# Performance work log

Measured on AMD Instinct MI355X. Metric: run time of the kernel, lower is better.

The kernel has to match this reference:

```python
import jax, jax.numpy as jnp
import numpy as np

B, N, D = 2, 2048, 128
DEPTH, RECURRENCE = 3, 3
EDGE_P = 0.03  # Bernoulli edge density -> avg degree ~61


def _p(key, shape, fan_in):
    return jax.random.normal(key, shape, dtype=jnp.float32) / np.float32(np.sqrt(fan_in))


def setup_inputs() -> dict:
    key = jax.random.key(0)
    ks = jax.random.split(key, 6)
    node = jax.random.normal(ks[0], (B, N, 1), dtype=jnp.float32)
    A = (jax.random.uniform(ks[1], (B, N, N)) < EDGE_P).astype(jnp.float32)
    edge = jax.random.uniform(ks[2], (B, N, N), dtype=jnp.float32) + 0.1  # strictly positive edge weights
    inp = {"node": node, "edge": edge, "A": A}
    # (fan_in, heads) per attention layer; last layer hardcodes heads=2, concat=False
    specs = [(1, 1), (D, 1), (D, 2)]
    for l, (fin, H) in enumerate(specs):
        kk = jax.random.split(ks[3 + l], 5)
        inp[f"Wq{l}"] = _p(kk[0], (fin, H, D), fin)
        inp[f"Wk{l}"] = _p(kk[1], (fin, H, D), fin)
        inp[f"Wv{l}"] = _p(kk[2], (fin, H, D), fin)
        inp[f"We{l}"] = _p(kk[3], (H, D), 1)  # lin_edge: edge_dim=1 -> H*D, stored as (H, D)
        inp[f"Ws{l}"] = _p(kk[4], (fin, H * D if l < DEPTH - 1 else D), fin)  # root/skip lin
    return inp


def _layer_norm(x, eps=1e-5):
    mu = x.mean(-1, keepdims=True)
    var = ((x - mu) ** 2).mean(-1, keepdims=True)
    return (x - mu) / jnp.sqrt(var + eps)


def _tconv(x, e_t, mask, Wq, Wk, Wv, We, Ws, concat):
    # PyG TransformerConv (bias removed, root_weight=True):
    #   alpha_ij = softmax_j( q_i . (k_j + W_e e_ij) / sqrt(d) ) over in-neighbors j of i
    #   out_i = sum_j alpha_ij (v_j + W_e e_ij)  (+ W_skip x_i)
    # e_ij is a scalar so W_e e_ij = e_ij * We, a rank-1 term we never materialize per-edge.
    # x: (b,n,fin); e_t[b,dst,src]; We: (H,d)
    H, d = We.shape
    q = jnp.einsum('bnf,fhd->bnhd', x, Wq)
    k = jnp.einsum('bnf,fhd->bnhd', x, Wk)
    v = jnp.einsum('bnf,fhd->bnhd', x, Wv)
    scores = jnp.einsum('bihd,bjhd->bhij', q, k)  # i=dst, j=src
    qe = jnp.einsum('bihd,hd->bhi', q, We)
    scores = (scores + qe[..., None] * e_t[:, None]) / np.float32(np.sqrt(d))
    scores = jnp.where(mask[:, None], scores, jnp.finfo(scores.dtype).min)
    alpha = jax.nn.softmax(scores, axis=-1)
    alpha = jnp.where(mask[:, None], alpha, 0.0)  # isolated dst nodes aggregate to zero
    out = jnp.einsum('bhij,bjhd->bihd', alpha, v)
    ew = jnp.einsum('bhij,bij->bhi', alpha, e_t)  # sum_j alpha * e_ij
    out = out + ew.transpose(0, 2, 1)[..., None] * We
    out = out.reshape(x.shape[0], x.shape[1], H * d) if concat else out.mean(axis=2)
    return out + x @ Ws


def reference(node, edge, A, Wq0, Wk0, Wv0, We0, Ws0, Wq1, Wk1, Wv1, We1, Ws1, Wq2, Wk2, Wv2, We2, Ws2):
    e = edge * A
    e_t = jnp.swapaxes(e, 1, 2)  # e_t[b, dst, src]  (edge_index: row=src, col=dst)
    mask = e_t != 0  # dense_to_sparse keeps nonzero entries
    layers = [
        (Wq0, Wk0, Wv0, We0, Ws0, True),
        (Wq1, Wk1, Wv1, We1, Ws1, True),
        (Wq2, Wk2, Wv2, We2, Ws2, False),
    ]
    emb = node
    for r in range(RECURRENCE):
        for l in range(DEPTH):
            if r != 0 and l == 0:
                continue
            Wq, Wk, Wv, We, Ws, concat = layers[l]
            emb = _tconv(emb, e_t, mask, Wq, Wk, Wv, We, Ws, concat)
            if l != DEPTH - 1:
                emb = jax.nn.relu(_layer_norm(emb))
    return emb  # (b, n, out_dim[-1])
```

## Files before the change

### kernel.cpp

```cpp
#include <hip/hip_runtime.h>
#include <hip/hip_bf16.h>

#define BB 2
#define NN 2048
#define DD 128
#define BN (BB*NN)
#define CAP 128
#define TD 16
#define QSTR 256
#define SSTR 128
#define INV_SQRT_D 0.08838834764831845f

typedef __attribute__((ext_vector_type(8))) short short8;
typedef __attribute__((ext_vector_type(4))) float f32x4;

__device__ inline float b2f(unsigned short u) {
    union { unsigned int i; float f; } c; c.i = (unsigned int)u << 16; return c.f;
}
__device__ inline float b2f_hi(unsigned int raw) {
    union { unsigned int i; float f; } c; c.i = raw & 0xffff0000u; return c.f;
}
__device__ inline float b2f_lo(unsigned int raw) {
    union { unsigned int i; float f; } c; c.i = raw << 16; return c.f;
}

__global__ __launch_bounds__(256) void prep(
    const float* __restrict__ A, const float* __restrict__ edge,
    const float* __restrict__ node,
    const float* __restrict__ Wq0, const float* __restrict__ Wk0,
    const float* __restrict__ Wv0, const float* __restrict__ Ws0,
    const float* __restrict__ Wq1, const float* __restrict__ Wk1,
    const float* __restrict__ Wv1, const float* __restrict__ Ws1,
    const float* __restrict__ Wq2, const float* __restrict__ Wk2,
    const float* __restrict__ Wv2, const float* __restrict__ Ws2,
    __hip_bfloat16* __restrict__ Wt1, __hip_bfloat16* __restrict__ Wt2,
    float* __restrict__ q, __hip_bfloat16* __restrict__ kA,
    __hip_bfloat16* __restrict__ vA, float* __restrict__ s,
    int* __restrict__ deg, unsigned short* __restrict__ cols,
    float* __restrict__ evals)
{
    __shared__ int   cnt[TD];
    __shared__ int   csh[TD][CAP];
    __shared__ float esh[TD][CAP];
    __shared__ float xnode[16];

    int bid = blockIdx.x;
    int tid = threadIdx.x;

    if (bid < 256) {
        int b    = bid >> 7;
        int dst0 = (bid & 127) * TD;

        if (tid < TD) cnt[tid] = 0;
        __syncthreads();

        int srcOff = tid >> 2;
        int dOff   = (tid & 3) * 4;
        const size_t base = (size_t)b * NN * NN + dst0 + dOff;

#pragma unroll 2
        for (int s0 = 0; s0 < NN; s0 += 64) {
            int src = s0 + srcOff;
            float4 a4 = *(const float4*)&A[base + (size_t)src * NN];
            float4 e4 = *(const float4*)&edge[base + (size_t)src * NN];
            int gsrc = b * NN + src;
            float av[4] = {a4.x, a4.y, a4.z, a4.w};
            float ev[4] = {e4.x, e4.y, e4.z, e4.w};
#pragma unroll
            for (int u = 0; u < 4; u++) {
                if (av[u] != 0.f) {
                    int d = dOff + u;
                    int slot = atomicAdd(&cnt[d], 1);
                    if (slot < CAP) { csh[d][slot] = gsrc; esh[d][slot] = ev[u] * av[u]; }
                }
            }
        }
        __syncthreads();

        if (tid < TD) deg[b * NN + dst0 + tid] = min(cnt[tid], CAP);
        for (int idx = tid; idx < TD * CAP; idx += 256) {
            int d = idx / CAP, i = idx % CAP;
            if (i < min(cnt[d], CAP)) {
                size_t row = (size_t)(b * NN + dst0 + d);
                cols [row * CAP + i] = (unsigned short)csh[d][i];
                evals[row * CAP + i] = esh[d][i];
            }
        }
    } else if (bid < 256 + 1408) {
        int c = bid - 256;
        if (tid < DD) {
            const float *Wq, *Wk, *Wv, *Ws; __hip_bfloat16* Wt; int n, HD;
            if (c < 512) { Wq = Wq1; Wk = Wk1; Wv = Wv1; Ws = Ws1; Wt = Wt1; n = c;       HD = DD;     }
            else         { Wq = Wq2; Wk = Wk2; Wv = Wv2; Ws = Ws2; Wt = Wt2; n = c - 512; HD = 2 * DD; }
            const float* src; int ld; int col;
            if      (n < HD)     { src = Wq; col = n;          ld = HD; }
            else if (n < 2*HD)   { src = Wk; col = n - HD;     ld = HD; }
            else if (n < 3*HD)   { src = Wv; col = n - 2*HD;   ld = HD; }
            else                 { src = Ws; col = n - 3*HD;   ld = DD; }
            Wt[(size_t)n * DD + tid] = __float2bfloat16(src[(size_t)tid * ld + col]);
        }
    } else {
        int row0 = (bid - (256 + 1408)) * 16;
        if (tid < 16) xnode[tid] = node[row0 + tid];
        __syncthreads();
        for (int i = tid; i < TD * 512; i += 256) {
            int r = i >> 9, col = i & 511;
            float xv = xnode[r];
            if (col < DD) {
                q[(size_t)(row0 + r) * QSTR + col] = xv * Wq0[col];
            } else if (col < 2*DD) {
                int lc = col - DD;
                kA[(size_t)(row0 + r) * 256 + lc] = __float2bfloat16(xv * Wk0[lc]);
            } else if (col < 3*DD) {
                int lc = col - 2*DD;
                vA[(size_t)(row0 + r) * 256 + lc] = __float2bfloat16(xv * Wv0[lc]);
            } else {
                int lc = col - 3*DD;
                s[(size_t)(row0 + r) * SSTR + lc] = xv * Ws0[lc];
            }
        }
    }
}

template<int H, bool MEANH, bool LNRELU, int NCOLS, int HDN, int KVSI, int KVSO>
__global__ __launch_bounds__(1024) void fused_attn(
    float* qio,
    const __hip_bfloat16* __restrict__ k,
    const __hip_bfloat16* __restrict__ v,
    float* sio,
    const int* __restrict__ deg,
    const unsigned short* __restrict__ cols,
    const float* __restrict__ evals, const float* __restrict__ We,
    const __hip_bfloat16* __restrict__ Wt,
    __hip_bfloat16* __restrict__ kn, __hip_bfloat16* __restrict__ vn,
    float* __restrict__ out)
{
    const int HD = H * DD;
    int wid  = threadIdx.x >> 6;
    int lane = threadIdx.x & 63;
    int row0 = blockIdx.x * 16;
    int row  = row0 + wid;
    int sub  = lane >> 4;
    int s    = lane & 15;
    int c0   = lane * 2;

    __shared__ int            jc_s[16][CAP];
    __shared__ float          ev_s[16][CAP];
    __shared__ __hip_bfloat16 xs[16][136];
    int*   jc = jc_s[wid];
    float* ev = ev_s[wid];

    int dg = min(deg[row], CAP);
    for (int m = lane; m < dg; m += 64) {
        jc[m] = (int)cols[(size_t)row * CAP + m];
        ev[m] = evals[(size_t)row * CAP + m];
    }

    float qh[H][8];
    float qeI[H];
#pragma unroll
    for (int h = 0; h < H; h++) {
        const float* qp = &qio[(size_t)row * QSTR + h * DD + s * 8];
        const float* wp = &We[h * DD + s * 8];
        float pe = 0.f;
#pragma unroll
        for (int t = 0; t < 8; t++) { qh[h][t] = qp[t]; pe += qp[t] * wp[t]; }
#pragma unroll
        for (int off = 1; off < 16; off <<= 1) pe += __shfl_xor(pe, off);
        qeI[h] = pe * INV_SQRT_D;
    }

    float l_acc[H], ew_acc[H], acc[H][2];
#pragma unroll
    for (int h = 0; h < H; h++) { l_acc[h] = 0.f; ew_acc[h] = 0.f; acc[h][0] = 0.f; acc[h][1] = 0.f; }

    for (int m0 = 0; m0 < dg; m0 += 8) {
        int   e0  = m0 + sub,       e1  = m0 + 4 + sub;
        bool  ok0 = e0 < dg,        ok1 = e1 < dg;
        int   ec0 = ok0 ? e0 : m0,  ec1 = ok1 ? e1 : m0;
        int   j0  = jc[ec0],        j1  = jc[ec1];
        float ee0 = ev[ec0],        ee1 = ev[ec1];

        int jb[8];
#pragma unroll
        for (int es = 0; es < 8; es++) jb[es] = jc[(m0 + es < dg) ? m0 + es : m0];

        unsigned int vraw[H][8];
#pragma unroll
        for (int h = 0; h < H; h++)
#pragma unroll
            for (int es = 0; es < 8; es++)
                vraw[h][es] = *(const unsigned int*)&v[(size_t)jb[es] * KVSI + h * DD + c0];
        short8 kk0[H], kk1[H];
#pragma unroll
        for (int h = 0; h < H; h++) {
            kk0[h] = *(const short8*)&k[(size_t)j0 * KVSI + h * DD + s * 8];
            kk1[h] = *(const short8*)&k[(size_t)j1 * KVSI + h * DD + s * 8];
        }

#pragma unroll
        for (int h = 0; h < H; h++) {
            float p0 = qh[h][0]*b2f((unsigned short)kk0[h][0]) + qh[h][1]*b2f((unsigned short)kk0[h][1])
                     + qh[h][2]*b2f((unsigned short)kk0[h][2]) + qh[h][3]*b2f((unsigned short)kk0[h][3])
                     + qh[h][4]*b2f((unsigned short)kk0[h][4]) + qh[h][5]*b2f((unsigned short)kk0[h][5])
                     + qh[h][6]*b2f((unsigned short)kk0[h][6]) + qh[h][7]*b2f((unsigned short)kk0[h][7]);
            float p1 = qh[h][0]*b2f((unsigned short)kk1[h][0]) + qh[h][1]*b2f((unsigned short)kk1[h][1])
                     + qh[h][2]*b2f((unsigned short)kk1[h][2]) + qh[h][3]*b2f((unsigned short)kk1[h][3])
                     + qh[h][4]*b2f((unsigned short)kk1[h][4]) + qh[h][5]*b2f((unsigned short)kk1[h][5])
                     + qh[h][6]*b2f((unsigned short)kk1[h][6]) + qh[h][7]*b2f((unsigned short)kk1[h][7]);
#pragma unroll
            for (int off = 1; off < 16; off <<= 1) {
                p0 += __shfl_xor(p0, off);
                p1 += __shfl_xor(p1, off);
            }
            float sc0 = ok0 ? (p0 * INV_SQRT_D + qeI[h] * ee0) : -1e30f;
            float sc1 = ok1 ? (p1 * INV_SQRT_D + qeI[h] * ee1) : -1e30f;
            float a0 = __expf(fminf(sc0, 60.f));
            float a1 = __expf(fminf(sc1, 60.f));
            l_acc[h]  += a0 + a1;
            ew_acc[h] += a0 * ee0 + a1 * ee1;
            float al0[4], al1[4];
#pragma unroll
            for (int es = 0; es < 4; es++) { al0[es] = __shfl(a0, es * 16); al1[es] = __shfl(a1, es * 16); }
#pragma unroll
            for (int es = 0; es < 4; es++) {
                acc[h][0] += al0[es] * b2f_lo(vraw[h][es]) + al1[es] * b2f_lo(vraw[h][es + 4]);
                acc[h][1] += al0[es] * b2f_hi(vraw[h][es]) + al1[es] * b2f_hi(vraw[h][es + 4]);
            }
        }
    }

    float rh[H][2];
#pragma unroll
    for (int h = 0; h < H; h++) {
        float l  = l_acc[h]  + __shfl_xor(l_acc[h], 16);
        float ew = ew_acc[h] + __shfl_xor(ew_acc[h], 16);
        l  += __shfl_xor(l, 32);
        ew += __shfl_xor(ew, 32);
        float invZ = (l > 0.f) ? 1.f / l : 0.f;
        rh[h][0] = (acc[h][0] + ew * We[h * DD + c0])     * invZ;
        rh[h][1] = (acc[h][1] + ew * We[h * DD + c0 + 1]) * invZ;
    }
    float r0, r1;
    if constexpr (MEANH) {
        r0 = 0.5f * (rh[0][0] + rh[H - 1][0]);
        r1 = 0.5f * (rh[0][1] + rh[H - 1][1]);
    } else {
        r0 = rh[0][0]; r1 = rh[0][1];
    }
    float2 sk = *(const float2*)&sio[(size_t)row * SSTR + c0];
    r0 += sk.x; r1 += sk.y;

    if constexpr (LNRELU) {
        float sum = r0 + r1, sq = r0 * r0 + r1 * r1;
#pragma unroll
        for (int off = 32; off; off >>= 1) { sum += __shfl_xor(sum, off); sq += __shfl_xor(sq, off); }
        float mu  = sum * (1.f / DD);
        float var = sq * (1.f / DD) - mu * mu;
        float rs  = rsqrtf(var + 1e-5f);
        r0 = fmaxf((r0 - mu) * rs, 0.f);
        r1 = fmaxf((r1 - mu) * rs, 0.f);
    }

    if constexpr (NCOLS == 0) {
        float2 res; res.x = r0; res.y = r1;
        *(float2*)&out[(size_t)row * DD + c0] = res;
    } else {
        __hip_bfloat162 o;
        o.x = __float2bfloat16(r0);
        o.y = __float2bfloat16(r1);
        *(__hip_bfloat162*)&xs[wid][c0] = o;
        __syncthreads();

        int m16 = lane & 15, quad = lane >> 4;
        short8 a[4];
#pragma unroll
        for (int ks = 0; ks < 4; ks++)
            a[ks] = *(const short8*)&xs[m16][ks * 32 + quad * 8];

#pragma unroll 1
        for (int tile = wid; tile < NCOLS / 16; tile += 16) {
            int n0 = tile * 16;
            f32x4 pacc = {0.f, 0.f, 0.f, 0.f};
#pragma unroll
            for (int ks = 0; ks < 4; ks++) {
                const short8* bp = (const short8*)&Wt[(size_t)(n0 + m16) * DD + ks * 32 + quad * 8];
                pacc = __builtin_amdgcn_mfma_f32_16x16x32_bf16(a[ks], *bp, pacc, 0, 0, 0);
            }
            if (n0 < HDN) {
#pragma unroll
                for (int r = 0; r < 4; r++)
                    qio[(size_t)(row0 + quad * 4 + r) * QSTR + n0 + m16] = pacc[r];
            } else if (n0 < 2*HDN) {
                int lc = n0 - HDN;
#pragma unroll
                for (int r = 0; r < 4; r++)
                    kn[(size_t)(row0 + quad * 4 + r) * KVSO + lc + m16] = __float2bfloat16(pacc[r]);
            } else if (n0 < 3*HDN) {
                int lc = n0 - 2*HDN;
#pragma unroll
                for (int r = 0; r < 4; r++)
                    vn[(size_t)(row0 + quad * 4 + r) * KVSO + lc + m16] = __float2bfloat16(pacc[r]);
            } else {
                int lc = n0 - 3*HDN;
#pragma unroll
                for (int r = 0; r < 4; r++)
                    sio[(size_t)(row0 + quad * 4 + r) * SSTR + lc + m16] = pacc[r];
            }
        }
    }
}

extern "C" void kernel_launch(void* const* d_in, const int* in_sizes, int n_in,
                              void* d_out, int out_size, void* d_ws, size_t ws_size,
                              hipStream_t stream)
{
    const float* node = (const float*)d_in[0];
    const float* edge = (const float*)d_in[1];
    const float* A    = (const float*)d_in[2];
    const float* Wq[3] = {(const float*)d_in[3],  (const float*)d_in[8],  (const float*)d_in[13]};
    const float* Wk[3] = {(const float*)d_in[4],  (const float*)d_in[9],  (const float*)d_in[14]};
    const float* Wv[3] = {(const float*)d_in[5],  (const float*)d_in[10], (const float*)d_in[15]};
    const float* We[3] = {(const float*)d_in[6],  (const float*)d_in[11], (const float*)d_in[16]};
    const float* Ws[3] = {(const float*)d_in[7],  (const float*)d_in[12], (const float*)d_in[17]};

    char* p = (char*)d_ws;
    float*          q  = (float*)p;          p += (size_t)BN * QSTR * 4;
    float*          s  = (float*)p;          p += (size_t)BN * SSTR * 4;
    __hip_bfloat16* kA = (__hip_bfloat16*)p; p += (size_t)BN * 256 * 2;
    __hip_bfloat16* vA = (__hip_bfloat16*)p; p += (size_t)BN * 256 * 2;
    __hip_bfloat16* kB = (__hip_bfloat16*)p; p += (size_t)BN * 128 * 2;
    __hip_bfloat16* vB = (__hip_bfloat16*)p; p += (size_t)BN * 128 * 2;
    __hip_bfloat16* Wt1 = (__hip_bfloat16*)p; p += (size_t)512 * DD * 2;
    __hip_bfloat16* Wt2 = (__hip_bfloat16*)p; p += (size_t)896 * DD * 2;
    int*            degb = (int*)p;            p += (size_t)BN * 4;
    float*          evb  = (float*)p;          p += (size_t)BN * CAP * 4;
    unsigned short* colb = (unsigned short*)p; p += (size_t)BN * CAP * 2;

    prep<<<256 + 1408 + BN / 16, 256, 0, stream>>>(
        A, edge, node,
        Wq[0], Wk[0], Wv[0], Ws[0],
        Wq[1], Wk[1], Wv[1], Ws[1],
        Wq[2], Wk[2], Wv[2], Ws[2],
        Wt1, Wt2, q, kA, vA, s, degb, colb, evb);

    fused_attn<1, false, true, 512, 128, 256, 128><<<BN / 16, 1024, 0, stream>>>(
        q, kA, vA, s, degb, colb, evb, We[0], Wt1, kB, vB, nullptr);
    fused_attn<1, false, true, 896, 256, 128, 256><<<BN / 16, 1024, 0, stream>>>(
        q, kB, vB, s, degb, colb, evb, We[1], Wt2, kA, vA, nullptr);
    fused_attn<2, true, false, 512, 128, 256, 128><<<BN / 16, 1024, 0, stream>>>(
        q, kA, vA, s, degb, colb, evb, We[2], Wt1, kB, vB, nullptr);
    fused_attn<1, false, true, 896, 256, 128, 256><<<BN / 16, 1024, 0, stream>>>(
        q, kB, vB, s, degb, colb, evb, We[1], Wt2, kA, vA, nullptr);
    fused_attn<2, true, false, 512, 128, 256, 128><<<BN / 16, 1024, 0, stream>>>(
        q, kA, vA, s, degb, colb, evb, We[2], Wt1, kB, vB, nullptr);
    fused_attn<1, false, true, 896, 256, 128, 256><<<BN / 16, 1024, 0, stream>>>(
        q, kB, vB, s, degb, colb, evb, We[1], Wt2, kA, vA, nullptr);
    fused_attn<2, true, false, 0, 0, 256, 0><<<BN / 16, 1024, 0, stream>>>(
        q, kA, vA, s, degb, colb, evb, We[2], nullptr, nullptr, nullptr, (float*)d_out);
}
```

Baseline: 320.9 us.

## Halve attention block to 8 rows and double-buffer neighbor K/V gathers

Shrinks each fused attention block from 16 to 8 destination rows (512 threads) and pads the MFMA projection input with zeroed rows, so only half the MFMA output rows are stored. It also software-pipelines the neighbor loop, loading the next 8 neighbors' K/V rows into a second register set while computing on the current set. The goal is more blocks per GPU and hiding gather latency. The cost is higher register pressure from the doubled buffers and wasted MFMA work on the padding rows.

```diff
diff --git a/kernel.cpp b/kernel.cpp
--- a/kernel.cpp
+++ b/kernel.cpp
@@ -123,7 +123,7 @@
 }
 
 template<int H, bool MEANH, bool LNRELU, int NCOLS, int HDN, int KVSI, int KVSO>
-__global__ __launch_bounds__(1024) void fused_attn(
+__global__ __launch_bounds__(512) void fused_attn(
     float* qio,
     const __hip_bfloat16* __restrict__ k,
     const __hip_bfloat16* __restrict__ v,
@@ -138,17 +138,22 @@
     const int HD = H * DD;
     int wid  = threadIdx.x >> 6;
     int lane = threadIdx.x & 63;
-    int row0 = blockIdx.x * 16;
+    int row0 = blockIdx.x * 8;
     int row  = row0 + wid;
     int sub  = lane >> 4;
     int s    = lane & 15;
     int c0   = lane * 2;
 
-    __shared__ int            jc_s[16][CAP];
-    __shared__ float          ev_s[16][CAP];
+    __shared__ int            jc_s[8][CAP];
+    __shared__ float          ev_s[8][CAP];
     __shared__ __hip_bfloat16 xs[16][136];
     int*   jc = jc_s[wid];
     float* ev = ev_s[wid];
+
+    if constexpr (NCOLS != 0) {
+        short* xz = (short*)&xs[8][0];
+        for (int i = threadIdx.x; i < 8 * 136; i += 512) xz[i] = 0;
+    }
 
     int dg = min(deg[row], CAP);
     for (int m = lane; m < dg; m += 64) {
@@ -174,30 +179,27 @@
 #pragma unroll
     for (int h = 0; h < H; h++) { l_acc[h] = 0.f; ew_acc[h] = 0.f; acc[h][0] = 0.f; acc[h][1] = 0.f; }
 
-    for (int m0 = 0; m0 < dg; m0 += 8) {
-        int   e0  = m0 + sub,       e1  = m0 + 4 + sub;
-        bool  ok0 = e0 < dg,        ok1 = e1 < dg;
-        int   ec0 = ok0 ? e0 : m0,  ec1 = ok1 ? e1 : m0;
-        int   j0  = jc[ec0],        j1  = jc[ec1];
-        float ee0 = ev[ec0],        ee1 = ev[ec1];
-
+    auto LOAD = [&](unsigned int (&vraw)[H][8], short8 (&kk0)[H], short8 (&kk1)[H], int base) {
         int jb[8];
 #pragma unroll
-        for (int es = 0; es < 8; es++) jb[es] = jc[(m0 + es < dg) ? m0 + es : m0];
-
-        unsigned int vraw[H][8];
+        for (int es = 0; es < 8; es++) jb[es] = jc[(base + es < dg) ? base + es : base];
 #pragma unroll
         for (int h = 0; h < H; h++)
 #pragma unroll
             for (int es = 0; es < 8; es++)
                 vraw[h][es] = *(const unsigned int*)&v[(size_t)jb[es] * KVSI + h * DD + c0];
-        short8 kk0[H], kk1[H];
+        int j0 = jb[sub], j1 = jb[4 + sub];
 #pragma unroll
         for (int h = 0; h < H; h++) {
             kk0[h] = *(const short8*)&k[(size_t)j0 * KVSI + h * DD + s * 8];
             kk1[h] = *(const short8*)&k[(size_t)j1 * KVSI + h * DD + s * 8];
         }
-
+    };
+    auto COMPUTE = [&](unsigned int (&vraw)[H][8], short8 (&kk0)[H], short8 (&kk1)[H], int base) {
+        int   e0  = base + sub,      e1  = base + 4 + sub;
+        bool  ok0 = e0 < dg,         ok1 = e1 < dg;
+        float ee0 = ev[ok0 ? e0 : base];
+        float ee1 = ev[ok1 ? e1 : base];
 #pragma unroll
         for (int h = 0; h < H; h++) {
             float p0 = qh[h][0]*b2f((unsigned short)kk0[h][0]) + qh[h][1]*b2f((unsigned short)kk0[h][1])
@@ -228,6 +230,26 @@
                 acc[h][1] += al0[es] * b2f_hi(vraw[h][es]) + al1[es] * b2f_hi(vraw[h][es + 4]);
             }
         }
+    };
+
+    unsigned int vrA[H][8], vrB[H][8];
+    short8 k0A[H], k1A[H], k0B[H], k1B[H];
+
+    if (dg > 0) {
+        LOAD(vrA, k0A, k1A, 0);
+        int m0 = 0;
+        while (true) {
+            int nx = m0 + 8;
+            if (nx < dg) LOAD(vrB, k0B, k1B, nx);
+            COMPUTE(vrA, k0A, k1A, m0);
+            m0 = nx;
+            if (m0 >= dg) break;
+            nx = m0 + 8;
+            if (nx < dg) LOAD(vrA, k0A, k1A, nx);
+            COMPUTE(vrB, k0B, k1B, m0);
+            m0 = nx;
+            if (m0 >= dg) break;
+        }
     }
 
     float rh[H][2];
@@ -279,7 +301,7 @@
             a[ks] = *(const short8*)&xs[m16][ks * 32 + quad * 8];
 
 #pragma unroll 1
-        for (int tile = wid; tile < NCOLS / 16; tile += 16) {
+        for (int tile = wid; tile < NCOLS / 16; tile += 8) {
             int n0 = tile * 16;
             f32x4 pacc = {0.f, 0.f, 0.f, 0.f};
 #pragma unroll
@@ -287,25 +309,27 @@
                 const short8* bp = (const short8*)&Wt[(size_t)(n0 + m16) * DD + ks * 32 + quad * 8];
                 pacc = __builtin_amdgcn_mfma_f32_16x16x32_bf16(a[ks], *bp, pacc, 0, 0, 0);
             }
-            if (n0 < HDN) {
-#pragma unroll
-                for (int r = 0; r < 4; r++)
-                    qio[(size_t)(row0 + quad * 4 + r) * QSTR + n0 + m16] = pacc[r];
-            } else if (n0 < 2*HDN) {
-                int lc = n0 - HDN;
-#pragma unroll
-                for (int r = 0; r < 4; r++)
-                    kn[(size_t)(row0 + quad * 4 + r) * KVSO + lc + m16] = __float2bfloat16(pacc[r]);
-            } else if (n0 < 3*HDN) {
-                int lc = n0 - 2*HDN;
-#pragma unroll
-                for (int r = 0; r < 4; r++)
-                    vn[(size_t)(row0 + quad * 4 + r) * KVSO + lc + m16] = __float2bfloat16(pacc[r]);
-            } else {
-                int lc = n0 - 3*HDN;
-#pragma unroll
-                for (int r = 0; r < 4; r++)
-                    sio[(size_t)(row0 + quad * 4 + r) * SSTR + lc + m16] = pacc[r];
+            if (quad < 2) {
+                if (n0 < HDN) {
+#pragma unroll
+                    for (int r = 0; r < 4; r++)
+                        qio[(size_t)(row0 + quad * 4 + r) * QSTR + n0 + m16] = pacc[r];
+                } else if (n0 < 2*HDN) {
+                    int lc = n0 - HDN;
+#pragma unroll
+                    for (int r = 0; r < 4; r++)
+                        kn[(size_t)(row0 + quad * 4 + r) * KVSO + lc + m16] = __float2bfloat16(pacc[r]);
+                } else if (n0 < 3*HDN) {
+                    int lc = n0 - 2*HDN;
+#pragma unroll
+                    for (int r = 0; r < 4; r++)
+                        vn[(size_t)(row0 + quad * 4 + r) * KVSO + lc + m16] = __float2bfloat16(pacc[r]);
+                } else {
+                    int lc = n0 - 3*HDN;
+#pragma unroll
+                    for (int r = 0; r < 4; r++)
+                        sio[(size_t)(row0 + quad * 4 + r) * SSTR + lc + m16] = pacc[r];
+                }
             }
         }
     }
@@ -344,18 +368,18 @@
         Wq[2], Wk[2], Wv[2], Ws[2],
         Wt1, Wt2, q, kA, vA, s, degb, colb, evb);
 
-    fused_attn<1, false, true, 512, 128, 256, 128><<<BN / 16, 1024, 0, stream>>>(
+    fused_attn<1, false, true, 512, 128, 256, 128><<<BN / 8, 512, 0, stream>>>(
         q, kA, vA, s, degb, colb, evb, We[0], Wt1, kB, vB, nullptr);
-    fused_attn<1, false, true, 896, 256, 128, 256><<<BN / 16, 1024, 0, stream>>>(
+    fused_attn<1, false, true, 896, 256, 128, 256><<<BN / 8, 512, 0, stream>>>(
         q, kB, vB, s, degb, colb, evb, We[1], Wt2, kA, vA, nullptr);
-    fused_attn<2, true, false, 512, 128, 256, 128><<<BN / 16, 1024, 0, stream>>>(
+    fused_attn<2, true, false, 512, 128, 256, 128><<<BN / 8, 512, 0, stream>>>(
         q, kA, vA, s, degb, colb, evb, We[2], Wt1, kB, vB, nullptr);
-    fused_attn<1, false, true, 896, 256, 128, 256><<<BN / 16, 1024, 0, stream>>>(
+    fused_attn<1, false, true, 896, 256, 128, 256><<<BN / 8, 512, 0, stream>>>(
         q, kB, vB, s, degb, colb, evb, We[1], Wt2, kA, vA, nullptr);
-    fused_attn<2, true, false, 512, 128, 256, 128><<<BN / 16, 1024, 0, stream>>>(
+    fused_attn<2, true, false, 512, 128, 256, 128><<<BN / 8, 512, 0, stream>>>(
         q, kA, vA, s, degb, colb, evb, We[2], Wt1, kB, vB, nullptr);
-    fused_attn<1, false, true, 896, 256, 128, 256><<<BN / 16, 1024, 0, stream>>>(
+    fused_attn<1, false, true, 896, 256, 128, 256><<<BN / 8, 512, 0, stream>>>(
         q, kB, vB, s, degb, colb, evb, We[1], Wt2, kA, vA, nullptr);
-    fused_attn<2, true, false, 0, 0, 256, 0><<<BN / 16, 1024, 0, stream>>>(
+    fused_attn<2, true, false, 0, 0, 256, 0><<<BN / 8, 512, 0, stream>>>(
         q, kA, vA, s, degb, colb, evb, We[2], nullptr, nullptr, nullptr, (float*)d_out);
 }
```

Result: slower. 366.9 us (+14.3%).
